# Performance work log

Hardware: AMD Instinct MI355X
Metric: run time of the kernel (lower is better)

The kernel has to match this reference:

```python
import jax, jax.numpy as jnp
import numpy as np

N, F, H, C = 4096, 512, 8, 128
LEAKY_ALPHA = 0.2
MASK_VAL = -10e9  # spektral uses -10e9 * (1 - A)


def setup_inputs() -> dict:
    key = jax.random.key(0)
    k1, k2, k3, k4, k5 = jax.random.split(key, 5)
    X = jax.random.normal(k1, (N, F), dtype=jnp.float32)
    # sparse-ish binary adjacency with self loops (dense layout as the layer expects)
    A = (jax.random.uniform(k2, (N, N)) < 0.01).astype(jnp.float32)
    A = jnp.maximum(A, jnp.eye(N, dtype=jnp.float32))
    W = jax.random.normal(k3, (H, F, C), dtype=jnp.float32) * (1.0 / np.sqrt(F))
    a_self = jax.random.normal(k4, (H, C), dtype=jnp.float32) * (1.0 / np.sqrt(C))
    a_neigh = jax.random.normal(k5, (H, C), dtype=jnp.float32) * (1.0 / np.sqrt(C))
    bias = jnp.zeros((H, C), dtype=jnp.float32)
    return {"X": X, "A": A, "W": W, "a_self": a_self, "a_neigh": a_neigh, "bias": bias}


def reference(X, A, W, a_self, a_neigh, bias):
    # per-head feature projection: [H, N, C]
    feats = jnp.einsum("nf,hfc->hnc", X, W)
    # attention scores e_ij = LeakyReLU(a_self . h_i + a_neigh . h_j)
    s_self = jnp.einsum("hnc,hc->hn", feats, a_self)    # [H, N]
    s_neigh = jnp.einsum("hnc,hc->hn", feats, a_neigh)  # [H, N]
    dense = s_self[:, :, None] + s_neigh[:, None, :]    # [H, N, N]
    dense = jnp.where(dense > 0, dense, LEAKY_ALPHA * dense)
    # adjacency mask then row softmax (dropout_rate=0 -> identity)
    dense = dense + MASK_VAL * (1.0 - A)[None, :, :]
    coef = jax.nn.softmax(dense, axis=-1)               # [H, N, N]
    out = jnp.einsum("hnm,hmc->hnc", coef, feats)       # [H, N, C]
    out = out + bias[:, None, :]
    # concat heads: [N, H*C]
    out = jnp.transpose(out, (1, 0, 2)).reshape(N, H * C)
    return jax.nn.relu(out)
```

## Files before the change

### kernel.cpp

```cpp
#include <hip/hip_runtime.h>
#include <hip/hip_bf16.h>

#define GN 4096
#define GF 512
#define GH 8
#define GC 128
#define CAP 256
#define BK 64
#define XS 72

typedef __hip_bfloat16 bf16;
typedef unsigned short u16;
typedef __attribute__((ext_vector_type(8))) short bf16x8;
typedef __attribute__((ext_vector_type(4))) float f32x4;

static __device__ inline u16 f2u16(float x) {
    union { bf16 b; u16 u; } cv;
    cv.b = __float2bfloat16(x);
    return cv.u;
}

__global__ __launch_bounds__(256) void feats_kernel(
    const float* __restrict__ X, const float* __restrict__ W,
    const float* __restrict__ a_self, const float* __restrict__ a_neigh,
    bf16* __restrict__ featsb, float* __restrict__ s_self,
    float* __restrict__ s_neigh)
{
    __shared__ u16 sX[128 * XS];
    __shared__ u16 sW[128 * XS];

    int h   = blockIdx.x >> 5;
    int n0  = (blockIdx.x & 31) << 7;
    int tid = threadIdx.x;
    int lane = tid & 63, wv = tid >> 6;
    int lm = lane & 15, q = lane >> 4;

    const float* Xp = X + (size_t)n0 * GF;
    const float* Wh = W + (size_t)h * GF * GC;

    f32x4 acc[2][8];
#pragma unroll
    for (int mt = 0; mt < 2; ++mt)
#pragma unroll
        for (int nt = 0; nt < 8; ++nt)
            acc[mt][nt] = (f32x4){0.f, 0.f, 0.f, 0.f};

    for (int k0 = 0; k0 < GF; k0 += BK) {
        __syncthreads();
#pragma unroll
        for (int it = 0; it < 8; ++it) {
            int idx = it * 256 + tid;
            int row = idx >> 4, q4 = idx & 15;
            float4 v = *(const float4*)&Xp[(size_t)row * GF + k0 + q4 * 4];
            u16* d = &sX[row * XS + q4 * 4];
            d[0] = f2u16(v.x); d[1] = f2u16(v.y);
            d[2] = f2u16(v.z); d[3] = f2u16(v.w);
        }
#pragma unroll
        for (int it = 0; it < 8; ++it) {
            int idx = it * 256 + tid;
            int k = idx >> 5, n4 = idx & 31;
            float4 v = *(const float4*)&Wh[(size_t)(k0 + k) * GC + n4 * 4];
            sW[(n4 * 4 + 0) * XS + k] = f2u16(v.x);
            sW[(n4 * 4 + 1) * XS + k] = f2u16(v.y);
            sW[(n4 * 4 + 2) * XS + k] = f2u16(v.z);
            sW[(n4 * 4 + 3) * XS + k] = f2u16(v.w);
        }
        __syncthreads();

#pragma unroll
        for (int ks = 0; ks < BK; ks += 32) {
            bf16x8 af[2], bfr[8];
#pragma unroll
            for (int mt = 0; mt < 2; ++mt)
                af[mt] = *(const bf16x8*)&sX[(wv * 32 + mt * 16 + lm) * XS + ks + q * 8];
#pragma unroll
            for (int nt = 0; nt < 8; ++nt)
                bfr[nt] = *(const bf16x8*)&sW[(nt * 16 + lm) * XS + ks + q * 8];
#pragma unroll
            for (int mt = 0; mt < 2; ++mt)
#pragma unroll
                for (int nt = 0; nt < 8; ++nt)
                    acc[mt][nt] = __builtin_amdgcn_mfma_f32_16x16x32_bf16(
                        af[mt], bfr[nt], acc[mt][nt], 0, 0, 0);
        }
    }

    float aS[8], aN[8];
#pragma unroll
    for (int nt = 0; nt < 8; ++nt) {
        aS[nt] = a_self[h * GC + nt * 16 + lm];
        aN[nt] = a_neigh[h * GC + nt * 16 + lm];
    }
#pragma unroll
    for (int mt = 0; mt < 2; ++mt) {
        float vs[4] = {0.f, 0.f, 0.f, 0.f};
        float vn[4] = {0.f, 0.f, 0.f, 0.f};
        int rbase = n0 + wv * 32 + mt * 16 + q * 4;
#pragma unroll
        for (int nt = 0; nt < 8; ++nt) {
            f32x4 v = acc[mt][nt];
            int col = nt * 16 + lm;
#pragma unroll
            for (int r = 0; r < 4; ++r) {
                featsb[((size_t)h * GN + rbase + r) * GC + col] = __float2bfloat16(v[r]);
                vs[r] += v[r] * aS[nt];
                vn[r] += v[r] * aN[nt];
            }
        }
#pragma unroll
        for (int r = 0; r < 4; ++r) {
            for (int off = 1; off < 16; off <<= 1) {
                vs[r] += __shfl_xor(vs[r], off);
                vn[r] += __shfl_xor(vn[r], off);
            }
            if (lm == 0) {
                s_self[h * GN + rbase + r]  = vs[r];
                s_neigh[h * GN + rbase + r] = vn[r];
            }
        }
    }
}

__global__ __launch_bounds__(128) void csr_kernel(
    const float* __restrict__ A, int* __restrict__ deg,
    u16* __restrict__ lists)
{
    int i   = blockIdx.x;
    int tid = threadIdx.x;
    __shared__ int cnt;
    if (tid == 0) cnt = 0;
    __syncthreads();

    u16* row = lists + (size_t)i * CAP;
    const float4* Arow = (const float4*)(A + (size_t)i * GN);
    for (int qd = tid; qd < GN / 4; qd += 128) {
        float4 a = Arow[qd];
        int j = qd * 4;
        if (a.x > 0.5f) { int s = atomicAdd(&cnt, 1); if (s < CAP) row[s] = (u16)j; }
        if (a.y > 0.5f) { int s = atomicAdd(&cnt, 1); if (s < CAP) row[s] = (u16)(j + 1); }
        if (a.z > 0.5f) { int s = atomicAdd(&cnt, 1); if (s < CAP) row[s] = (u16)(j + 2); }
        if (a.w > 0.5f) { int s = atomicAdd(&cnt, 1); if (s < CAP) row[s] = (u16)(j + 3); }
    }
    __syncthreads();
    if (tid == 0) deg[i] = cnt < CAP ? cnt : CAP;
}

__global__ __launch_bounds__(128) void attn_kernel(
    const int* __restrict__ deg, const u16* __restrict__ lists,
    const float* __restrict__ bias, const bf16* __restrict__ featsb,
    const float* __restrict__ s_self, const float* __restrict__ s_neigh,
    float* __restrict__ out)
{
    int h   = blockIdx.x >> 12;
    int i   = blockIdx.x & (GN - 1);
    int tid = threadIdx.x;
    int c   = tid;

    __shared__ int   jidx[CAP];
    __shared__ float p[CAP];
    __shared__ float redbuf[2];

    int M = deg[i];
    const u16* row = lists + (size_t)i * CAP;
    for (int k = tid; k < M; k += 128) jidx[k] = row[k];
    __syncthreads();

    float ssi = s_self[h * GN + i];
    const float* snh = s_neigh + h * GN;
    for (int k = tid; k < M; k += 128) {
        float e = ssi + snh[jidx[k]];
        p[k] = e > 0.f ? e : 0.2f * e;
    }
    __syncthreads();

    int lane = tid & 63, wv = tid >> 6;

    float m = -1e30f;
    for (int k = tid; k < M; k += 128) m = fmaxf(m, p[k]);
    for (int off = 32; off > 0; off >>= 1) m = fmaxf(m, __shfl_down(m, off));
    if (lane == 0) redbuf[wv] = m;
    __syncthreads();
    m = fmaxf(redbuf[0], redbuf[1]);
    __syncthreads();

    float s = 0.f;
    for (int k = tid; k < M; k += 128) {
        float e = __expf(p[k] - m);
        p[k] = e;
        s += e;
    }
    for (int off = 32; off > 0; off >>= 1) s += __shfl_down(s, off);
    __syncthreads();
    if (lane == 0) redbuf[wv] = s;
    __syncthreads();
    float inv = 1.f / (redbuf[0] + redbuf[1]);

    const bf16* fh = featsb + (size_t)h * GN * GC + c;
    float acc = 0.f;
    int k = 0;
    for (; k + 4 <= M; k += 4) {
        int   j0 = jidx[k],     j1 = jidx[k + 1];
        int   j2 = jidx[k + 2], j3 = jidx[k + 3];
        float p0 = p[k],        p1 = p[k + 1];
        float p2 = p[k + 2],    p3 = p[k + 3];
        acc += p0 * __bfloat162float(fh[(size_t)j0 * GC])
             + p1 * __bfloat162float(fh[(size_t)j1 * GC])
             + p2 * __bfloat162float(fh[(size_t)j2 * GC])
             + p3 * __bfloat162float(fh[(size_t)j3 * GC]);
    }
    for (; k < M; ++k) acc += p[k] * __bfloat162float(fh[(size_t)jidx[k] * GC]);

    float r = acc * inv + bias[h * GC + c];
    out[(size_t)i * (GH * GC) + h * GC + c] = fmaxf(r, 0.f);
}

extern "C" void kernel_launch(void* const* d_in, const int* in_sizes, int n_in,
                              void* d_out, int out_size, void* d_ws, size_t ws_size,
                              hipStream_t stream)
{
    const float* X       = (const float*)d_in[0];
    const float* A       = (const float*)d_in[1];
    const float* W       = (const float*)d_in[2];
    const float* a_self  = (const float*)d_in[3];
    const float* a_neigh = (const float*)d_in[4];
    const float* bias    = (const float*)d_in[5];
    float* out = (float*)d_out;

    bf16*  featsb  = (bf16*)d_ws;
    float* s_self  = (float*)(featsb + (size_t)GH * GN * GC);
    float* s_neigh = s_self + (size_t)GH * GN;
    int*   deg     = (int*)(s_neigh + (size_t)GH * GN);
    u16*   lists   = (u16*)(deg + GN);

    feats_kernel<<<GH * 32, 256, 0, stream>>>(X, W, a_self, a_neigh,
                                              featsb, s_self, s_neigh);
    csr_kernel<<<GN, 128, 0, stream>>>(A, deg, lists);
    attn_kernel<<<GH * GN, 128, 0, stream>>>(deg, lists, bias, featsb,
                                             s_self, s_neigh, out);
}
```

Baseline: 185.0 us.

## Halve feats tile rows, use ballot-based CSR build, pack attention gathers

The feature projection kernel now uses 64-row tiles, which doubles the block count to 512 and gives the GPU more parallelism. The CSR builder switches to 256-thread blocks and a wavefront ballot/popcount scheme, so it issues one shared atomic per wave per component instead of one atomic per nonzero. The attention aggregation packs probability and index into a float2, reads two bf16 channels per 32-bit load, splits neighbors across the two waves, and combines them through shared memory. These changes target atomic contention, under-filled feats launches and narrow gather loads, at the cost of an extra reduction step and less per-block reuse of W.

```diff
diff --git a/kernel.cpp b/kernel.cpp
--- a/kernel.cpp
+++ b/kernel.cpp
@@ -11,6 +11,7 @@
 
 typedef __hip_bfloat16 bf16;
 typedef unsigned short u16;
+typedef unsigned int u32;
 typedef __attribute__((ext_vector_type(8))) short bf16x8;
 typedef __attribute__((ext_vector_type(4))) float f32x4;
 
@@ -26,11 +27,11 @@
     bf16* __restrict__ featsb, float* __restrict__ s_self,
     float* __restrict__ s_neigh)
 {
-    __shared__ u16 sX[128 * XS];
+    __shared__ u16 sX[64 * XS];
     __shared__ u16 sW[128 * XS];
 
-    int h   = blockIdx.x >> 5;
-    int n0  = (blockIdx.x & 31) << 7;
+    int h   = blockIdx.x >> 6;
+    int n0  = (blockIdx.x & 63) << 6;
     int tid = threadIdx.x;
     int lane = tid & 63, wv = tid >> 6;
     int lm = lane & 15, q = lane >> 4;
@@ -38,17 +39,14 @@
     const float* Xp = X + (size_t)n0 * GF;
     const float* Wh = W + (size_t)h * GF * GC;
 
-    f32x4 acc[2][8];
-#pragma unroll
-    for (int mt = 0; mt < 2; ++mt)
-#pragma unroll
-        for (int nt = 0; nt < 8; ++nt)
-            acc[mt][nt] = (f32x4){0.f, 0.f, 0.f, 0.f};
+    f32x4 acc[8];
+#pragma unroll
+    for (int nt = 0; nt < 8; ++nt) acc[nt] = (f32x4){0.f, 0.f, 0.f, 0.f};
 
     for (int k0 = 0; k0 < GF; k0 += BK) {
         __syncthreads();
 #pragma unroll
-        for (int it = 0; it < 8; ++it) {
+        for (int it = 0; it < 4; ++it) {
             int idx = it * 256 + tid;
             int row = idx >> 4, q4 = idx & 15;
             float4 v = *(const float4*)&Xp[(size_t)row * GF + k0 + q4 * 4];
@@ -70,19 +68,15 @@
 
 #pragma unroll
         for (int ks = 0; ks < BK; ks += 32) {
-            bf16x8 af[2], bfr[8];
-#pragma unroll
-            for (int mt = 0; mt < 2; ++mt)
-                af[mt] = *(const bf16x8*)&sX[(wv * 32 + mt * 16 + lm) * XS + ks + q * 8];
+            bf16x8 af = *(const bf16x8*)&sX[(wv * 16 + lm) * XS + ks + q * 8];
+            bf16x8 bfr[8];
 #pragma unroll
             for (int nt = 0; nt < 8; ++nt)
                 bfr[nt] = *(const bf16x8*)&sW[(nt * 16 + lm) * XS + ks + q * 8];
 #pragma unroll
-            for (int mt = 0; mt < 2; ++mt)
-#pragma unroll
-                for (int nt = 0; nt < 8; ++nt)
-                    acc[mt][nt] = __builtin_amdgcn_mfma_f32_16x16x32_bf16(
-                        af[mt], bfr[nt], acc[mt][nt], 0, 0, 0);
+            for (int nt = 0; nt < 8; ++nt)
+                acc[nt] = __builtin_amdgcn_mfma_f32_16x16x32_bf16(
+                    af, bfr[nt], acc[nt], 0, 0, 0);
         }
     }
 
@@ -92,55 +86,68 @@
         aS[nt] = a_self[h * GC + nt * 16 + lm];
         aN[nt] = a_neigh[h * GC + nt * 16 + lm];
     }
-#pragma unroll
-    for (int mt = 0; mt < 2; ++mt) {
-        float vs[4] = {0.f, 0.f, 0.f, 0.f};
-        float vn[4] = {0.f, 0.f, 0.f, 0.f};
-        int rbase = n0 + wv * 32 + mt * 16 + q * 4;
-#pragma unroll
-        for (int nt = 0; nt < 8; ++nt) {
-            f32x4 v = acc[mt][nt];
-            int col = nt * 16 + lm;
-#pragma unroll
-            for (int r = 0; r < 4; ++r) {
-                featsb[((size_t)h * GN + rbase + r) * GC + col] = __float2bfloat16(v[r]);
-                vs[r] += v[r] * aS[nt];
-                vn[r] += v[r] * aN[nt];
-            }
-        }
+    float vs[4] = {0.f, 0.f, 0.f, 0.f};
+    float vn[4] = {0.f, 0.f, 0.f, 0.f};
+    int rbase = n0 + wv * 16 + q * 4;
+#pragma unroll
+    for (int nt = 0; nt < 8; ++nt) {
+        f32x4 v = acc[nt];
+        int col = nt * 16 + lm;
 #pragma unroll
         for (int r = 0; r < 4; ++r) {
-            for (int off = 1; off < 16; off <<= 1) {
-                vs[r] += __shfl_xor(vs[r], off);
-                vn[r] += __shfl_xor(vn[r], off);
-            }
-            if (lm == 0) {
-                s_self[h * GN + rbase + r]  = vs[r];
-                s_neigh[h * GN + rbase + r] = vn[r];
-            }
-        }
-    }
-}
-
-__global__ __launch_bounds__(128) void csr_kernel(
+            featsb[((size_t)h * GN + rbase + r) * GC + col] = __float2bfloat16(v[r]);
+            vs[r] += v[r] * aS[nt];
+            vn[r] += v[r] * aN[nt];
+        }
+    }
+#pragma unroll
+    for (int r = 0; r < 4; ++r) {
+        for (int off = 1; off < 16; off <<= 1) {
+            vs[r] += __shfl_xor(vs[r], off);
+            vn[r] += __shfl_xor(vn[r], off);
+        }
+        if (lm == 0) {
+            s_self[h * GN + rbase + r]  = vs[r];
+            s_neigh[h * GN + rbase + r] = vn[r];
+        }
+    }
+}
+
+__global__ __launch_bounds__(256) void csr_kernel(
     const float* __restrict__ A, int* __restrict__ deg,
     u16* __restrict__ lists)
 {
-    int i   = blockIdx.x;
-    int tid = threadIdx.x;
+    int i    = blockIdx.x;
+    int tid  = threadIdx.x;
+    int lane = tid & 63;
     __shared__ int cnt;
     if (tid == 0) cnt = 0;
     __syncthreads();
 
     u16* row = lists + (size_t)i * CAP;
     const float4* Arow = (const float4*)(A + (size_t)i * GN);
-    for (int qd = tid; qd < GN / 4; qd += 128) {
+    unsigned long long ltmask = (lane == 63) ? ~0ull >> 1
+                                             : (1ull << lane) - 1;
+#pragma unroll
+    for (int it = 0; it < 4; ++it) {
+        int qd = it * 256 + tid;
         float4 a = Arow[qd];
         int j = qd * 4;
-        if (a.x > 0.5f) { int s = atomicAdd(&cnt, 1); if (s < CAP) row[s] = (u16)j; }
-        if (a.y > 0.5f) { int s = atomicAdd(&cnt, 1); if (s < CAP) row[s] = (u16)(j + 1); }
-        if (a.z > 0.5f) { int s = atomicAdd(&cnt, 1); if (s < CAP) row[s] = (u16)(j + 2); }
-        if (a.w > 0.5f) { int s = atomicAdd(&cnt, 1); if (s < CAP) row[s] = (u16)(j + 3); }
+#pragma unroll
+        for (int comp = 0; comp < 4; ++comp) {
+            float av = comp == 0 ? a.x : comp == 1 ? a.y : comp == 2 ? a.z : a.w;
+            bool flag = av > 0.5f;
+            unsigned long long m = __ballot(flag);
+            if (m) {
+                int base = 0;
+                if (lane == 0) base = atomicAdd(&cnt, __popcll(m));
+                base = __shfl(base, 0);
+                if (flag) {
+                    int s = base + __popcll(m & ltmask);
+                    if (s < CAP) row[s] = (u16)(j + comp);
+                }
+            }
+        }
     }
     __syncthreads();
     if (tid == 0) deg[i] = cnt < CAP ? cnt : CAP;
@@ -155,29 +162,28 @@
     int h   = blockIdx.x >> 12;
     int i   = blockIdx.x & (GN - 1);
     int tid = threadIdx.x;
-    int c   = tid;
-
-    __shared__ int   jidx[CAP];
-    __shared__ float p[CAP];
-    __shared__ float redbuf[2];
+
+    __shared__ float2 pj[CAP];
+    __shared__ float  sacc[2][64][2];
+    __shared__ float  redbuf[2];
 
     int M = deg[i];
     const u16* row = lists + (size_t)i * CAP;
-    for (int k = tid; k < M; k += 128) jidx[k] = row[k];
+    for (int k = tid; k < M; k += 128) pj[k].y = __int_as_float((int)row[k]);
     __syncthreads();
 
     float ssi = s_self[h * GN + i];
     const float* snh = s_neigh + h * GN;
     for (int k = tid; k < M; k += 128) {
-        float e = ssi + snh[jidx[k]];
-        p[k] = e > 0.f ? e : 0.2f * e;
+        float e = ssi + snh[__float_as_int(pj[k].y)];
+        pj[k].x = e > 0.f ? e : 0.2f * e;
     }
     __syncthreads();
 
     int lane = tid & 63, wv = tid >> 6;
 
     float m = -1e30f;
-    for (int k = tid; k < M; k += 128) m = fmaxf(m, p[k]);
+    for (int k = tid; k < M; k += 128) m = fmaxf(m, pj[k].x);
     for (int off = 32; off > 0; off >>= 1) m = fmaxf(m, __shfl_down(m, off));
     if (lane == 0) redbuf[wv] = m;
     __syncthreads();
@@ -186,8 +192,8 @@
 
     float s = 0.f;
     for (int k = tid; k < M; k += 128) {
-        float e = __expf(p[k] - m);
-        p[k] = e;
+        float e = __expf(pj[k].x - m);
+        pj[k].x = e;
         s += e;
     }
     for (int off = 32; off > 0; off >>= 1) s += __shfl_down(s, off);
@@ -196,23 +202,29 @@
     __syncthreads();
     float inv = 1.f / (redbuf[0] + redbuf[1]);
 
-    const bf16* fh = featsb + (size_t)h * GN * GC + c;
-    float acc = 0.f;
-    int k = 0;
-    for (; k + 4 <= M; k += 4) {
-        int   j0 = jidx[k],     j1 = jidx[k + 1];
-        int   j2 = jidx[k + 2], j3 = jidx[k + 3];
-        float p0 = p[k],        p1 = p[k + 1];
-        float p2 = p[k + 2],    p3 = p[k + 3];
-        acc += p0 * __bfloat162float(fh[(size_t)j0 * GC])
-             + p1 * __bfloat162float(fh[(size_t)j1 * GC])
-             + p2 * __bfloat162float(fh[(size_t)j2 * GC])
-             + p3 * __bfloat162float(fh[(size_t)j3 * GC]);
-    }
-    for (; k < M; ++k) acc += p[k] * __bfloat162float(fh[(size_t)jidx[k] * GC]);
-
-    float r = acc * inv + bias[h * GC + c];
-    out[(size_t)i * (GH * GC) + h * GC + c] = fmaxf(r, 0.f);
+    int c2 = tid & 63;
+    const u32* fh = (const u32*)(featsb + (size_t)h * GN * GC) + c2;
+    float acc0 = 0.f, acc1 = 0.f;
+#pragma unroll 2
+    for (int k = wv; k < M; k += 2) {
+        float2 v = pj[k];
+        int j = __float_as_int(v.y);
+        u32 u = fh[(size_t)j << 6];
+        float lo = __uint_as_float(u << 16);
+        float hi = __uint_as_float(u & 0xffff0000u);
+        acc0 += v.x * lo;
+        acc1 += v.x * hi;
+    }
+    sacc[wv][c2][0] = acc0;
+    sacc[wv][c2][1] = acc1;
+    __syncthreads();
+
+    if (tid < 64) {
+        float r0 = (sacc[0][tid][0] + sacc[1][tid][0]) * inv + bias[h * GC + 2 * tid];
+        float r1 = (sacc[0][tid][1] + sacc[1][tid][1]) * inv + bias[h * GC + 2 * tid + 1];
+        float2* op = (float2*)&out[(size_t)i * (GH * GC) + h * GC + 2 * tid];
+        *op = make_float2(fmaxf(r0, 0.f), fmaxf(r1, 0.f));
+    }
 }
 
 extern "C" void kernel_launch(void* const* d_in, const int* in_sizes, int n_in,
@@ -233,9 +245,9 @@
     int*   deg     = (int*)(s_neigh + (size_t)GH * GN);
     u16*   lists   = (u16*)(deg + GN);
 
-    feats_kernel<<<GH * 32, 256, 0, stream>>>(X, W, a_self, a_neigh,
+    feats_kernel<<<GH * 64, 256, 0, stream>>>(X, W, a_self, a_neigh,
                                               featsb, s_self, s_neigh);
-    csr_kernel<<<GN, 128, 0, stream>>>(A, deg, lists);
+    csr_kernel<<<GN, 256, 0, stream>>>(A, deg, lists);
     attn_kernel<<<GH * GN, 128, 0, stream>>>(deg, lists, bias, featsb,
                                              s_self, s_neigh, out);
 }
```

Measured after the change: 201.6 us. +8.9%, slower.
